# Performance work log

Hardware: AMD Instinct MI355X
Metric: run time of the kernel (lower is better)

Reference implementation:

```python
import jax, jax.numpy as jnp
import numpy as np

B = 16384
NUM_CLASS = 1000
IGNORE_INDEX = -100


def setup_inputs() -> dict:
    key = jax.random.key(0)
    k0, k1, k2, k3, kt = jax.random.split(key, 5)
    return {
        "x0": jax.random.normal(k0, (B, NUM_CLASS), dtype=jnp.float32),
        "x1": jax.random.normal(k1, (B, NUM_CLASS), dtype=jnp.float32),
        "x2": jax.random.normal(k2, (B, NUM_CLASS), dtype=jnp.float32),
        "x3": jax.random.normal(k3, (B, NUM_CLASS), dtype=jnp.float32),
        "target": jax.random.randint(kt, (B,), 0, NUM_CLASS, dtype=jnp.int64)
        if jax.config.jax_enable_x64 else jax.random.randint(kt, (B,), 0, NUM_CLASS, dtype=jnp.int32),
    }


def reference(x0, x1, x2, x3, target):
    """Vectorized TopKBaseLoss.get_topk_targets.

    torch.topk(p, k=num_class) is a full descending argsort; the per-sample
    Python loop computes, for each row, the rank of the current target in
    that sorted order (or ignore_index if absent, e.g. already ignored).
    Stage 3's topk is computed but never used in the original, so we skip it.
    Returns the 4-element targets list: [target, t_after_stage0, t_after_stage1, t_after_stage2].
    """
    t = target
    outs = [target]
    for p in (x0, x1, x2):
        ind = jnp.argsort(-p, axis=-1)                 # [B, C] descending class order
        match = ind == t[:, None]                      # [B, C] membership mask
        found = jnp.any(match, axis=-1)                # [B]
        rank = jnp.argmax(match, axis=-1).astype(t.dtype)  # position of target in sorted order
        t = jnp.where(found, rank, jnp.asarray(IGNORE_INDEX, t.dtype))
        outs.append(t)
    return tuple(outs)
```

## Files before the change

kernel.cpp:

```cpp
#include <hip/hip_runtime.h>

#define BROWS 16384
#define NCLASS 1000
#define IGNORE_INDEX (-100)

__global__ __launch_bounds__(256) void TopKBaseLoss_80281528697452_kernel(
    const float* __restrict__ x0,
    const float* __restrict__ x1,
    const float* __restrict__ x2,
    const int*   __restrict__ target,
    int*         __restrict__ out)
{
    const int gid  = blockIdx.x * blockDim.x + threadIdx.x;
    const int row  = gid >> 6;
    const int lane = threadIdx.x & 63;
    if (row >= BROWS) return;

    int t = target[row];
    if (lane == 0) out[row] = t;

    const float* xs0 = x0 + (long)row * NCLASS;
    const float* xs1 = x1 + (long)row * NCLASS;
    const float* xs2 = x2 + (long)row * NCLASS;
    const float* stages[3] = {xs0, xs1, xs2};

    #pragma unroll
    for (int s = 0; s < 3; ++s) {
        int nt;
        if (t < 0 || t >= NCLASS) {
            nt = IGNORE_INDEX;
        } else {
            const float* __restrict__ x = stages[s];
            const float v = x[t];
            int cnt = 0;
            #pragma unroll 4
            for (int j = lane; j < NCLASS; j += 64) {
                const float xv = x[j];
                cnt += (xv > v) || (xv == v && j < t);
            }
            #pragma unroll
            for (int off = 32; off > 0; off >>= 1)
                cnt += __shfl_xor(cnt, off, 64);
            nt = cnt;
        }
        t = nt;
        if (lane == 0) out[(s + 1) * BROWS + row] = t;
    }
}

extern "C" void kernel_launch(void* const* d_in, const int* in_sizes, int n_in,
                              void* d_out, int out_size, void* d_ws, size_t ws_size,
                              hipStream_t stream) {
    const float* x0     = (const float*)d_in[0];
    const float* x1     = (const float*)d_in[1];
    const float* x2     = (const float*)d_in[2];
    const int*   target = (const int*)d_in[4];
    int*         out    = (int*)d_out;

    const int waves_per_block = 256 / 64;
    const int grid = (BROWS + waves_per_block - 1) / waves_per_block;
    TopKBaseLoss_80281528697452_kernel<<<grid, 256, 0, stream>>>(x0, x1, x2, target, out);
}
```

Before: 38.91 us.

## Preload all three stage rows as float4 and fetch target value via shuffle

```diff
diff --git a/kernel.cpp b/kernel.cpp
--- a/kernel.cpp
+++ b/kernel.cpp
@@ -1,7 +1,9 @@
 #include <hip/hip_runtime.h>
+#include <math.h>
 
 #define BROWS 16384
 #define NCLASS 1000
+#define NF4 250
 #define IGNORE_INDEX (-100)
 
 __global__ __launch_bounds__(256) void TopKBaseLoss_80281528697452_kernel(
@@ -16,27 +18,54 @@
     const int lane = threadIdx.x & 63;
     if (row >= BROWS) return;
 
-    int t = target[row];
-    if (lane == 0) out[row] = t;
+    const int t0 = target[row];
+    if (lane == 0) out[row] = t0;
 
-    const float* xs0 = x0 + (long)row * NCLASS;
-    const float* xs1 = x1 + (long)row * NCLASS;
-    const float* xs2 = x2 + (long)row * NCLASS;
-    const float* stages[3] = {xs0, xs1, xs2};
+    const float4* __restrict__ r0 = (const float4*)(x0 + (long)row * NCLASS);
+    const float4* __restrict__ r1 = (const float4*)(x1 + (long)row * NCLASS);
+    const float4* __restrict__ r2 = (const float4*)(x2 + (long)row * NCLASS);
 
+    const float NEG = -INFINITY;
+    const float4 pad = make_float4(NEG, NEG, NEG, NEG);
+
+    float4 d[3][4];
+    #pragma unroll
+    for (int k = 0; k < 4; ++k) {
+        const int idx4 = k * 64 + lane;
+        const bool ok = idx4 < NF4;
+        d[0][k] = ok ? r0[idx4] : pad;
+        d[1][k] = ok ? r1[idx4] : pad;
+        d[2][k] = ok ? r2[idx4] : pad;
+    }
+
+    int t = t0;
     #pragma unroll
     for (int s = 0; s < 3; ++s) {
         int nt;
         if (t < 0 || t >= NCLASS) {
             nt = IGNORE_INDEX;
         } else {
-            const float* __restrict__ x = stages[s];
-            const float v = x[t];
+            const int idx4 = t >> 2;
+            const int lane_src = idx4 & 63;
+            const int kt = idx4 >> 6;
+            const int et = t & 3;
+            const float4 dk = (kt == 0) ? d[s][0]
+                            : (kt == 1) ? d[s][1]
+                            : (kt == 2) ? d[s][2] : d[s][3];
+            const float cand = (et == 0) ? dk.x
+                             : (et == 1) ? dk.y
+                             : (et == 2) ? dk.z : dk.w;
+            const float v = __shfl(cand, lane_src, 64);
+
             int cnt = 0;
-            #pragma unroll 4
-            for (int j = lane; j < NCLASS; j += 64) {
-                const float xv = x[j];
-                cnt += (xv > v) || (xv == v && j < t);
+            #pragma unroll
+            for (int k = 0; k < 4; ++k) {
+                const int jb = (k * 64 + lane) * 4;
+                const float4 q = d[s][k];
+                cnt += (q.x > v) || (q.x == v && (jb + 0) < t);
+                cnt += (q.y > v) || (q.y == v && (jb + 1) < t);
+                cnt += (q.z > v) || (q.z == v && (jb + 2) < t);
+                cnt += (q.w > v) || (q.w == v && (jb + 3) < t);
             }
             #pragma unroll
             for (int off = 32; off > 0; off >>= 1)
```

New measurement: 100.5 us. +158.4%, slower.

## Prefetch all three stage rows as float4 registers and shuffle target value

Applied to the files above, without the earlier changes.

```diff
diff --git a/kernel.cpp b/kernel.cpp
--- a/kernel.cpp
+++ b/kernel.cpp
@@ -1,8 +1,41 @@
 #include <hip/hip_runtime.h>
+#include <math.h>
 
 #define BROWS 16384
 #define NCLASS 1000
+#define NF4 250
 #define IGNORE_INDEX (-100)
+
+__device__ __forceinline__ int rank_stage(float4 q0, float4 q1, float4 q2, float4 q3,
+                                          int t, int lane)
+{
+    const int idx4     = t >> 2;
+    const int lane_src = idx4 & 63;
+    const int kt       = idx4 >> 6;
+    const int et       = t & 3;
+    const float4 dk  = (kt == 0) ? q0 : (kt == 1) ? q1 : (kt == 2) ? q2 : q3;
+    const float cand = (et == 0) ? dk.x : (et == 1) ? dk.y : (et == 2) ? dk.z : dk.w;
+    const float v = __shfl(cand, lane_src, 64);
+
+    const int j0 = (lane)       * 4;
+    const int j1 = (64  + lane) * 4;
+    const int j2 = (128 + lane) * 4;
+    const int j3 = (192 + lane) * 4;
+
+    int cnt = 0;
+#define CNT4(Q, JB)                                          \
+    cnt += ((Q).x > v) || ((Q).x == v && ((JB) + 0) < t);    \
+    cnt += ((Q).y > v) || ((Q).y == v && ((JB) + 1) < t);    \
+    cnt += ((Q).z > v) || ((Q).z == v && ((JB) + 2) < t);    \
+    cnt += ((Q).w > v) || ((Q).w == v && ((JB) + 3) < t);
+    CNT4(q0, j0) CNT4(q1, j1) CNT4(q2, j2) CNT4(q3, j3)
+#undef CNT4
+
+    #pragma unroll
+    for (int off = 32; off > 0; off >>= 1)
+        cnt += __shfl_xor(cnt, off, 64);
+    return cnt;
+}
 
 __global__ __launch_bounds__(256) void TopKBaseLoss_80281528697452_kernel(
     const float* __restrict__ x0,
@@ -16,36 +49,36 @@
     const int lane = threadIdx.x & 63;
     if (row >= BROWS) return;
 
-    int t = target[row];
-    if (lane == 0) out[row] = t;
+    const int t0 = target[row];
+    if (lane == 0) out[row] = t0;
 
-    const float* xs0 = x0 + (long)row * NCLASS;
-    const float* xs1 = x1 + (long)row * NCLASS;
-    const float* xs2 = x2 + (long)row * NCLASS;
-    const float* stages[3] = {xs0, xs1, xs2};
+    const float4* __restrict__ r0 = (const float4*)(x0 + (long)row * NCLASS);
+    const float4* __restrict__ r1 = (const float4*)(x1 + (long)row * NCLASS);
+    const float4* __restrict__ r2 = (const float4*)(x2 + (long)row * NCLASS);
 
-    #pragma unroll
-    for (int s = 0; s < 3; ++s) {
-        int nt;
-        if (t < 0 || t >= NCLASS) {
-            nt = IGNORE_INDEX;
-        } else {
-            const float* __restrict__ x = stages[s];
-            const float v = x[t];
-            int cnt = 0;
-            #pragma unroll 4
-            for (int j = lane; j < NCLASS; j += 64) {
-                const float xv = x[j];
-                cnt += (xv > v) || (xv == v && j < t);
-            }
-            #pragma unroll
-            for (int off = 32; off > 0; off >>= 1)
-                cnt += __shfl_xor(cnt, off, 64);
-            nt = cnt;
-        }
-        t = nt;
-        if (lane == 0) out[(s + 1) * BROWS + row] = t;
-    }
+    const float NEG = -INFINITY;
+    const float4 pad = make_float4(NEG, NEG, NEG, NEG);
+
+    const int i0 = lane, i1 = 64 + lane, i2 = 128 + lane, i3 = 192 + lane;
+    const bool ok3 = (i3 < NF4);
+
+    float4 a0 = r0[i0], a1 = r0[i1], a2 = r0[i2], a3 = ok3 ? r0[i3] : pad;
+    float4 b0 = r1[i0], b1 = r1[i1], b2 = r1[i2], b3 = ok3 ? r1[i3] : pad;
+    float4 c0 = r2[i0], c1 = r2[i1], c2 = r2[i2], c3 = ok3 ? r2[i3] : pad;
+
+    int t = t0;
+
+    if (t >= 0 && t < NCLASS) t = rank_stage(a0, a1, a2, a3, t, lane);
+    else                      t = IGNORE_INDEX;
+    if (lane == 0) out[BROWS + row] = t;
+
+    if (t >= 0 && t < NCLASS) t = rank_stage(b0, b1, b2, b3, t, lane);
+    else                      t = IGNORE_INDEX;
+    if (lane == 0) out[2 * BROWS + row] = t;
+
+    if (t >= 0 && t < NCLASS) t = rank_stage(c0, c1, c2, c3, t, lane);
+    else                      t = IGNORE_INDEX;
+    if (lane == 0) out[3 * BROWS + row] = t;
 }
 
 extern "C" void kernel_launch(void* const* d_in, const int* in_sizes, int n_in,
```

Result: faster. 35.76 us (-8.1%).
